# Optimization experiments

Measured on AMD Instinct MI355X. Metric: run time of the kernel, lower is better.

## Reference

```python
import jax, jax.numpy as jnp
import numpy as np

H = 128  # hidden_size hard-coded in the torch module


def _lin(key, fan_in, shape):
    b = 1.0 / np.sqrt(fan_in)
    return jax.random.uniform(key, shape, minval=-b, maxval=b, dtype=jnp.float32)


def _gru_step(x, wih, bih, bhh):
    # torch GRU, single time step, h0 = 0; gate order (r, z, n)
    g = x @ wih.T + bih
    xr, xz, xn = jnp.split(g, 3, axis=-1)
    br, bz, bn = jnp.split(bhh, 3)
    r = jax.nn.sigmoid(xr + br)
    z = jax.nn.sigmoid(xz + bz)
    n = jnp.tanh(xn + r * bn)
    return (1.0 - z) * n  # h' = (1-z)*n + z*0


def _forward(x_node, x_edge, nt_w1, nt_b1, nt_w2, nt_b2, et_w, et_b,
             ngru_wih, ngru_bih, ngru_bhh, egru_wih, egru_bih, egru_bhh,
             natt_w, natt_b, eatt_w, eatt_b,
             lr_w1, lr_b1, lr_w2, lr_b2, cr_w1, cr_b1, cr_w2, cr_b2,
             mr_w1, mr_b1, mr_w2, mr_b2, pairs):
    B, N, _ = x_node.shape
    node_f = jax.nn.relu(x_node @ nt_w1 + nt_b1) @ nt_w2 + nt_b2      # [B,N,H]
    edge_f = x_edge @ et_w + et_b                                      # [B,N,N,H]
    nh = eh = None
    for _ in range(2):  # num_time_steps; GRU inputs are NOT updated in the original loop
        nh = _gru_step(node_f, ngru_wih, ngru_bih, ngru_bhh)           # [B,N,H]
        eh = _gru_step(edge_f, egru_wih, egru_bih, egru_bhh)           # [B,N,N,H]
        # --- node message pooling: attention over column index j ---
        n_col = jnp.broadcast_to(nh[:, :, None, :], eh.shape)          # aug[b,i,j] = nh[b,i]
        logits = (jnp.concatenate([n_col, eh], -1) @ natt_w)[..., 0] + natt_b[0]
        w = jax.nn.softmax(logits, axis=-1)                            # [B,N,N]
        nh = jnp.einsum('bijk,bij->bik', eh, w)                        # pooled node states
        # --- edge message pooling: 2-way attention over (row, col) node states ---
        n_row = jnp.broadcast_to(nh[:, None, :, :], eh.shape)          # [b,i,j] = nh[b,j]
        n_col = jnp.broadcast_to(nh[:, :, None, :], eh.shape)          # [b,i,j] = nh[b,i]
        l_row = (jnp.concatenate([n_row, eh], -1) @ eatt_w)[..., 0] + eatt_b[0]
        l_col = (jnp.concatenate([n_col, eh], -1) @ eatt_w)[..., 0] + eatt_b[0]
        w2 = jax.nn.softmax(jnp.stack([l_row, l_col], -1), axis=-1)    # [B,N,N,2]
        eh = w2[..., 0:1] * n_row + w2[..., 1:2] * n_col               # einsum('bijl,bijkl->bijk')
    # --- classifier inputs (aggregator = elementwise mean) ---
    i0, i1 = pairs[..., 0], pairs[..., 1]                              # [B,P]
    emb0 = jnp.take_along_axis(nh, i0[..., None], axis=1)              # [B,P,H]
    emb1 = jnp.take_along_axis(nh, i1[..., None], axis=1)
    bix = jnp.arange(B)[:, None]
    e01 = eh[bix, i0, i1]                                              # [B,P,H]
    e10 = eh[bix, i1, i0]
    ci = jnp.concatenate([(emb0 + emb1) * 0.5, (e01 + e10) * 0.5], -1)  # [B,P,2H]

    def head(w1, b1, wo, bo):
        return jax.nn.relu(ci @ w1 + b1) @ wo + bo

    lr = head(lr_w1, lr_b1, lr_w2, lr_b2)
    cr = head(cr_w1, cr_b1, cr_w2, cr_b2)
    mr = head(mr_w1, mr_b1, mr_w2, mr_b2)
    return jnp.concatenate([lr, cr, mr], axis=-1)                      # [B,P,6+5+3]


def setup_inputs() -> dict:
    B, N, P = 16, 64, 128
    NF, EF = 1024, 512
    CH = 512  # classifier hidden
    ks = list(jax.random.split(jax.random.key(0), 40))
    k = iter(ks)
    inp = {}
    inp['concatenated_node_features'] = jax.random.normal(next(k), (B, N, NF), dtype=jnp.float32)
    inp['interaction_feature'] = jax.random.normal(next(k), (B, N, N, EF), dtype=jnp.float32)
    inp['nt_w1'] = _lin(next(k), NF, (NF, 512)); inp['nt_b1'] = _lin(next(k), NF, (512,))
    inp['nt_w2'] = _lin(next(k), 512, (512, H)); inp['nt_b2'] = _lin(next(k), 512, (H,))
    inp['et_w'] = _lin(next(k), EF, (EF, H)); inp['et_b'] = _lin(next(k), EF, (H,))
    inp['ngru_wih'] = _lin(next(k), H, (3 * H, H))
    inp['ngru_bih'] = _lin(next(k), H, (3 * H,)); inp['ngru_bhh'] = _lin(next(k), H, (3 * H,))
    inp['egru_wih'] = _lin(next(k), H, (3 * H, H))
    inp['egru_bih'] = _lin(next(k), H, (3 * H,)); inp['egru_bhh'] = _lin(next(k), H, (3 * H,))
    inp['natt_w'] = _lin(next(k), 2 * H, (2 * H, 1)); inp['natt_b'] = _lin(next(k), 2 * H, (1,))
    inp['eatt_w'] = _lin(next(k), 2 * H, (2 * H, 1)); inp['eatt_b'] = _lin(next(k), 2 * H, (1,))
    for name, od in (('lr', 6), ('cr', 5), ('mr', 3)):
        inp[name + '_w1'] = _lin(next(k), 2 * H, (2 * H, CH))
        inp[name + '_b1'] = _lin(next(k), 2 * H, (CH,))
        inp[name + '_w2'] = _lin(next(k), CH, (CH, od))
        inp[name + '_b2'] = _lin(next(k), CH, (od,))
    inp['object_pairs'] = jax.random.randint(next(k), (B, P, 2), 0, N, dtype=jnp.int64 if jax.config.jax_enable_x64 else jnp.int32)
    inp['num_relation'] = jax.random.randint(next(k), (B,), 0, P, dtype=jnp.int64 if jax.config.jax_enable_x64 else jnp.int32)
    return inp


def reference(concatenated_node_features, interaction_feature,
              nt_w1, nt_b1, nt_w2, nt_b2, et_w, et_b,
              ngru_wih, ngru_bih, ngru_bhh, egru_wih, egru_bih, egru_bhh,
              natt_w, natt_b, eatt_w, eatt_b,
              lr_w1, lr_b1, lr_w2, lr_b2, cr_w1, cr_b1, cr_w2, cr_b2,
              mr_w1, mr_b1, mr_w2, mr_b2, object_pairs, num_relation):
    # num_relation is read but unused in the original make_classifier_inputs loop
    return _forward(concatenated_node_features, interaction_feature,
                    nt_w1, nt_b1, nt_w2, nt_b2, et_w, et_b,
                    ngru_wih, ngru_bih, ngru_bhh, egru_wih, egru_bih, egru_bhh,
                    natt_w, natt_b, eatt_w, eatt_b,
                    lr_w1, lr_b1, lr_w2, lr_b2, cr_w1, cr_b1, cr_w2, cr_b2,
                    mr_w1, mr_b1, mr_w2, mr_b2, object_pairs)
```

## Files before the change

### kernel.cpp

```cpp
#include <hip/hip_runtime.h>
#include <math.h>
#include <stdint.h>


typedef __attribute__((ext_vector_type(8))) short short8;
typedef __attribute__((ext_vector_type(4))) float f32x4;

#define DEVINL __device__ __forceinline__

DEVINL float sigmoidf_(float x) { return 1.0f / (1.0f + __expf(-x)); }
DEVINL float tanhf_(float x) {
    float e = __expf(2.0f * x);
    return (e - 1.0f) / (e + 1.0f);
}
DEVINL short bf16_rne(float f) {
    uint32_t u = __float_as_uint(f);
    u += 0x7FFFu + ((u >> 16) & 1u);
    return (short)(u >> 16);
}
DEVINL float bf16_to_f(short s) {
    return __uint_as_float(((uint32_t)(uint16_t)s) << 16);
}
DEVINL void gload_lds16(const void* g, void* l) {
    __builtin_amdgcn_global_load_lds(
        (const __attribute__((address_space(1))) void*)(uintptr_t)g,
        (__attribute__((address_space(3))) void*)(uint32_t)(uintptr_t)l,
        16, 0, 0);
}
DEVINL void ldsbar() {
    asm volatile("s_waitcnt lgkmcnt(0)\n\ts_barrier" ::: "memory");
    __builtin_amdgcn_sched_barrier(0);
}

__global__ __launch_bounds__(256) void prep_all(
    const float* __restrict__ et_w, const float* __restrict__ wih,
    const float* __restrict__ w1a, const float* __restrict__ w1b,
    const float* __restrict__ w1c,
    short* __restrict__ Bf1, short* __restrict__ Bf2,
    short* __restrict__ Wf1_hi, short* __restrict__ Wf1_lo)
{
    const int bid = blockIdx.x, t = threadIdx.x;
    if (bid < 256) {
        int idx = bid * 256 + t;
        int k = idx >> 7, n = idx & 127;
        float v = et_w[(size_t)k * 128 + n];
        short hi = bf16_rne(v), lo = bf16_rne(v - bf16_to_f(hi));
        int kt = k >> 5, ct = n >> 4;
        int lane = (((k >> 3) & 3) << 4) | (n & 15);
        int j = k & 7;
        size_t s0 = ((((size_t)kt * 2 + 0) * 8 + ct) * 64 + lane) * 8 + j;
        size_t s1 = ((((size_t)kt * 2 + 1) * 8 + ct) * 64 + lane) * 8 + j;
        Bf1[s0] = hi; Bf1[s1] = lo;
    } else if (bid < 448) {
        int idx = (bid - 256) * 256 + t;
        int n = idx >> 7, k = idx & 127;
        float v = wih[(size_t)n * 128 + k];
        short hi = bf16_rne(v), lo = bf16_rne(v - bf16_to_f(hi));
        int kt = k >> 5, ct = n >> 4;
        int lane = (((k >> 3) & 3) << 4) | (n & 15);
        int j = k & 7;
        size_t s0 = ((((size_t)kt * 2 + 0) * 24 + ct) * 64 + lane) * 8 + j;
        size_t s1 = ((((size_t)kt * 2 + 1) * 24 + ct) * 64 + lane) * 8 + j;
        Bf2[s0] = hi; Bf2[s1] = lo;
    } else {
        int idx = (bid - 448) * 256 + t;
        int h = idx >> 17;
        int r = idx & 131071;
        int k = r >> 9, c = r & 511;
        const float* w1 = (h == 0) ? w1a : (h == 1) ? w1b : w1c;
        float v = w1[(size_t)k * 512 + c];
        short hi = bf16_rne(v), lo = bf16_rne(v - bf16_to_f(hi));
        int kt = k >> 5, ct = c >> 4;
        int lane = (((k >> 3) & 3) << 4) | (c & 15);
        int j = k & 7;
        size_t fidx = ((((size_t)h * 8 + kt) * 32 + ct) * 64 + lane) * 8 + j;
        Wf1_hi[fidx] = hi;
        Wf1_lo[fidx] = lo;
    }
}

#define PH1_ITER(KT, BH0, BH1, BL0, BL1, NBH0, NBH1, NBL0, NBL1,              \
                 PCV0, PCV1, PLD0, PLD1, RBUF, WBUF)                          \
    {                                                                         \
        if ((KT) < 15) {                                                      \
            const short* bkt = Bf1 + (size_t)((KT) + 1) * 8192;               \
            NBH0 = *(const short8*)(bkt + ct0 * 512 + ln8);                   \
            NBH1 = *(const short8*)(bkt + ct1 * 512 + ln8);                   \
            NBL0 = *(const short8*)(bkt + 4096 + ct0 * 512 + ln8);            \
            NBL1 = *(const short8*)(bkt + 4096 + ct1 * 512 + ln8);            \
            float av[8] = {PCV0.x, PCV0.y, PCV0.z, PCV0.w,                    \
                           PCV1.x, PCV1.y, PCV1.z, PCV1.w};                   \
            short8 h8, l8;                                                    \
            _Pragma("unroll") for (int j = 0; j < 8; ++j) {                   \
                short h = bf16_rne(av[j]);                                    \
                h8[j] = h;                                                    \
                l8[j] = bf16_rne(av[j] - bf16_to_f(h));                       \
            }                                                                 \
            *(short8*)(smem + (WBUF) + aslotb) = h8;                          \
            *(short8*)(smem + (WBUF) + 4096 + aslotb) = l8;                   \
        }                                                                     \
        if ((KT) < 14) {                                                      \
            PLD0 = *(const float4*)(aptr + (size_t)((KT) + 2) * 32);          \
            PLD1 = *(const float4*)(aptr + (size_t)((KT) + 2) * 32 + 4);      \
        }                                                                     \
        {                                                                     \
            const char* Ah_c = smem + (RBUF);                                 \
            short8 Ahf[4], Alf[4];                                            \
            _Pragma("unroll") for (int rt = 0; rt < 4; ++rt) {                \
                Ahf[rt] = *(const short8*)(Ah_c + (rt * 64 + lane) * 16);     \
                Alf[rt] = *(const short8*)(Ah_c + 4096 + (rt * 64 + lane) * 16); \
            }                                                                 \
            _Pragma("unroll") for (int rt = 0; rt < 4; ++rt) {                \
                acc1[rt][0] = __builtin_amdgcn_mfma_f32_16x16x32_bf16(Ahf[rt], BH0, acc1[rt][0], 0, 0, 0); \
                acc1[rt][0] = __builtin_amdgcn_mfma_f32_16x16x32_bf16(Alf[rt], BH0, acc1[rt][0], 0, 0, 0); \
                acc1[rt][0] = __builtin_amdgcn_mfma_f32_16x16x32_bf16(Ahf[rt], BL0, acc1[rt][0], 0, 0, 0); \
                acc1[rt][1] = __builtin_amdgcn_mfma_f32_16x16x32_bf16(Ahf[rt], BH1, acc1[rt][1], 0, 0, 0); \
                acc1[rt][1] = __builtin_amdgcn_mfma_f32_16x16x32_bf16(Alf[rt], BH1, acc1[rt][1], 0, 0, 0); \
                acc1[rt][1] = __builtin_amdgcn_mfma_f32_16x16x32_bf16(Ahf[rt], BL1, acc1[rt][1], 0, 0, 0); \
            }                                                                 \
        }                                                                     \
        ldsbar();                                                             \
    }

__global__ __launch_bounds__(256, 2) void fused_kernel(
    const float* __restrict__ x_edge,
    const short* __restrict__ Bf1, const short* __restrict__ Bf2,
    const float* __restrict__ et_b,
    const float* __restrict__ bih, const float* __restrict__ bhh,
    const float* __restrict__ natt_w, const float* __restrict__ eatt_w,
    float* __restrict__ nh_p, float* __restrict__ u_out)
{
    __shared__ __align__(16) char smem[81920];
    const int t = threadIdx.x;
    const int wv = t >> 6, lane = t & 63;
    const int g = blockIdx.x;
    const size_t bm = (size_t)g * 64;

    const int arow = t >> 2, akb = t & 3;
    const int aslotb = (((arow >> 4) * 64) + ((akb << 4) | (arow & 15))) * 16;
    const float* aptr = x_edge + (bm + arow) * 512 + akb * 8;

    const int ct0 = wv * 2, ct1 = wv * 2 + 1;
    const int ln8 = lane * 8;

    f32x4 acc1[4][2] = {};

    float4 paA0, paA1, paB0, paB1;
    short8 bhA0, bhA1, blA0, blA1, bhB0, bhB1, blB0, blB1;

    paA0 = *(const float4*)(aptr);
    paA1 = *(const float4*)(aptr + 4);
    paB0 = *(const float4*)(aptr + 32);
    paB1 = *(const float4*)(aptr + 36);
    {
        const short* bkt = Bf1;
        bhA0 = *(const short8*)(bkt + ct0 * 512 + ln8);
        bhA1 = *(const short8*)(bkt + ct1 * 512 + ln8);
        blA0 = *(const short8*)(bkt + 4096 + ct0 * 512 + ln8);
        blA1 = *(const short8*)(bkt + 4096 + ct1 * 512 + ln8);
    }
    {
        float av[8] = {paA0.x, paA0.y, paA0.z, paA0.w,
                       paA1.x, paA1.y, paA1.z, paA1.w};
        short8 h8, l8;
#pragma unroll
        for (int j = 0; j < 8; ++j) {
            short h = bf16_rne(av[j]);
            h8[j] = h;
            l8[j] = bf16_rne(av[j] - bf16_to_f(h));
        }
        *(short8*)(smem + aslotb) = h8;
        *(short8*)(smem + 4096 + aslotb) = l8;
    }
    ldsbar();

    for (int kt = 0; kt < 16; kt += 2) {
        PH1_ITER(kt, bhA0, bhA1, blA0, blA1, bhB0, bhB1, blB0, blB1,
                 paB0, paB1, paA0, paA1, 0, 8192)
        PH1_ITER(kt + 1, bhB0, bhB1, blB0, blB1, bhA0, bhA1, blA0, blA1,
                 paA0, paA1, paB0, paB1, 8192, 0)
    }
    __syncthreads();

    float* ef_s = (float*)smem;
#pragma unroll
    for (int c = 0; c < 2; ++c) {
        int col = wv * 32 + c * 16 + (lane & 15);
        float bias = et_b[col];
#pragma unroll
        for (int rt = 0; rt < 4; ++rt) {
#pragma unroll
            for (int q = 0; q < 4; ++q) {
                int row = rt * 16 + ((lane >> 4) << 2) + q;
                ef_s[row * 132 + col] = acc1[rt][c][q] + bias;
            }
        }
    }
    __syncthreads();

    short* AF = (short*)(smem + 49152);
#pragma unroll
    for (int u2 = 0; u2 < 4; ++u2) {
        int unit = t + u2 * 256;
        int kt2 = unit >> 8;
        int rt = (unit >> 6) & 3;
        int ln = unit & 63;
        int row = rt * 16 + (ln & 15);
        int feat0 = kt2 * 32 + (ln >> 4) * 8;
        const float* src = ef_s + row * 132 + feat0;
        float4 v0 = *(const float4*)(src);
        float4 v1 = *(const float4*)(src + 4);
        float av[8] = {v0.x, v0.y, v0.z, v0.w, v1.x, v1.y, v1.z, v1.w};
        short8 h8, l8;
#pragma unroll
        for (int j = 0; j < 8; ++j) {
            short hh = bf16_rne(av[j]);
            h8[j] = hh;
            l8[j] = bf16_rne(av[j] - bf16_to_f(hh));
        }
        *(short8*)(AF + (((kt2 * 2 + 0) * 4 + rt) * 64 + ln) * 8) = h8;
        *(short8*)(AF + (((kt2 * 2 + 1) * 4 + rt) * 64 + ln) * 8) = l8;
    }
    __syncthreads();

    f32x4 acc[4][6] = {};
    for (int kt = 0; kt < 4; ++kt) {
        {
            const char* src = (const char*)Bf2 + (size_t)kt * 49152;
#pragma unroll
            for (int i = 0; i < 12; ++i) {
                int off = (t + i * 256) * 16;
                gload_lds16(src + off, smem + off);
            }
        }
        __syncthreads();

        const char* Ab = (const char*)AF + kt * 8192;
        short8 Ahf[4], Alf[4];
#pragma unroll
        for (int rt = 0; rt < 4; ++rt) {
            Ahf[rt] = *(const short8*)(Ab + (rt * 64 + lane) * 16);
            Alf[rt] = *(const short8*)(Ab + 4096 + (rt * 64 + lane) * 16);
        }
#pragma unroll
        for (int c = 0; c < 6; ++c) {
            int ctg = ((c >> 1) << 3) + (wv << 1) + (c & 1);
            short8 Bh = *(const short8*)(smem + (ctg * 64 + lane) * 16);
            short8 Bl = *(const short8*)(smem + 24576 + (ctg * 64 + lane) * 16);
#pragma unroll
            for (int rt = 0; rt < 4; ++rt) {
                acc[rt][c] = __builtin_amdgcn_mfma_f32_16x16x32_bf16(Ahf[rt], Bh, acc[rt][c], 0, 0, 0);
                acc[rt][c] = __builtin_amdgcn_mfma_f32_16x16x32_bf16(Alf[rt], Bh, acc[rt][c], 0, 0, 0);
                acc[rt][c] = __builtin_amdgcn_mfma_f32_16x16x32_bf16(Ahf[rt], Bl, acc[rt][c], 0, 0, 0);
            }
        }
        __syncthreads();
    }

    const int EHP = 132;
    float* eh_s = (float*)smem;
    float* red  = (float*)(smem + 33792);
    float* s2v  = red + 256;
    float* ewv  = s2v + 64;
#pragma unroll
    for (int cc = 0; cc < 2; ++cc) {
        int o = (wv << 5) + (cc << 4) + (lane & 15);
        float bco = bih[o] + bhh[o];
        float bcz = bih[128 + o] + bhh[128 + o];
        float bcn = bih[256 + o];
        float bn3 = bhh[256 + o];
#pragma unroll
        for (int rt = 0; rt < 4; ++rt) {
#pragma unroll
            for (int q = 0; q < 4; ++q) {
                int row = rt * 16 + ((lane >> 4) << 2) + q;
                float r = sigmoidf_(acc[rt][cc][q] + bco);
                float z = sigmoidf_(acc[rt][2 + cc][q] + bcz);
                float n = tanhf_(acc[rt][4 + cc][q] + bcn + r * bn3);
                eh_s[row * EHP + o] = (1.0f - z) * n;
            }
        }
    }
    __syncthreads();

    {
        int j = t >> 2, q = t & 3;
        const float* row = eh_s + j * EHP + q * 32;
        const float* wb = natt_w + 128 + q * 32;
        float a = 0.f;
#pragma unroll
        for (int k2 = 0; k2 < 32; ++k2) a = fmaf(row[k2], wb[k2], a);
        red[t] = a;
    }
    __syncthreads();
    if (t < 64) s2v[t] = red[4 * t] + red[4 * t + 1] + red[4 * t + 2] + red[4 * t + 3];
    __syncthreads();
    if (t < 64) {
        float m = -1e30f;
        for (int j = 0; j < 64; ++j) m = fmaxf(m, s2v[j]);
        ewv[t] = __expf(s2v[t] - m);
    }
    __syncthreads();
    float inv = 0.f;
    for (int j = 0; j < 64; ++j) inv += ewv[j];
    inv = 1.0f / inv;
    {
        int o = t & 127, h = t >> 7;
        float a = 0.f;
        for (int j = h * 32; j < h * 32 + 32; ++j)
            a = fmaf(ewv[j], eh_s[j * EHP + o], a);
        __syncthreads();
        red[t] = a;
    }
    __syncthreads();
    if (t < 128) {
        float v = (red[t] + red[t + 128]) * inv;
        nh_p[(size_t)g * 128 + t] = v;
        red[t] = v * eatt_w[t];
    }
    __syncthreads();
    for (int s = 64; s > 0; s >>= 1) {
        if (t < s) red[t] += red[t + s];
        __syncthreads();
    }
    if (t == 0) u_out[g] = red[0];
}

__global__ __launch_bounds__(128) void ci_kernel(
    const float* __restrict__ nh_p, const float* __restrict__ u,
    const int* __restrict__ pairs, float* __restrict__ ci)
{
    const int bp = blockIdx.x;
    const int b  = bp >> 7;
    const int t  = threadIdx.x;
    int i0 = pairs[bp * 2 + 0];
    int i1 = pairs[bp * 2 + 1];
    const float* n0 = nh_p + (size_t)(b * 64 + i0) * 128;
    const float* n1 = nh_p + (size_t)(b * 64 + i1) * 128;
    float s = sigmoidf_(u[b * 64 + i1] - u[b * 64 + i0]);
    float v0 = n0[t], v1 = n1[t];
    ci[(size_t)bp * 256 + t]       = 0.5f * (v0 + v1);
    ci[(size_t)bp * 256 + 128 + t] = s * v1 + (1.0f - s) * v0;
}

__global__ __launch_bounds__(256, 1) void headcls_kernel(
    const float* __restrict__ ci,
    const short* __restrict__ Wf1_hi, const short* __restrict__ Wf1_lo,
    const float* __restrict__ b1a, const float* __restrict__ b1b,
    const float* __restrict__ b1c,
    const float* __restrict__ w2a, const float* __restrict__ w2b,
    const float* __restrict__ w2c,
    const float* __restrict__ b2a, const float* __restrict__ b2b,
    const float* __restrict__ b2c,
    float* __restrict__ out)
{
    __shared__ __align__(16) char smem[139264];
    const int t = threadIdx.x;
    const int wv = t >> 6, lane = t & 63;
    const int rb = blockIdx.x;
    const int hd = blockIdx.y;
    const float* b1 = hd == 0 ? b1a : hd == 1 ? b1b : b1c;
    const float* w2 = hd == 0 ? w2a : hd == 1 ? w2b : w2c;
    const float* b2 = hd == 0 ? b2a : hd == 1 ? b2b : b2c;
    const int od  = hd == 0 ? 6 : hd == 1 ? 5 : 3;
    const int off = hd == 0 ? 0 : hd == 1 ? 6 : 11;

    const int arow = t >> 2, akb = t & 3;
    const int abyte = ((((arow >> 4) * 64) + ((akb << 4) | (arow & 15))) * 8) * 2;
    const float* aptr = ci + ((size_t)rb * 32 + arow) * 256 + akb * 8;

    f32x4 acc[2][8] = {};

    float4 a0, a1;
    if (t < 128) {
        a0 = *(const float4*)(aptr);
        a1 = *(const float4*)(aptr + 4);
    }
    {
        const char* sh = (const char*)(Wf1_hi + (size_t)hd * 8 * 32 * 512);
        const char* sl = (const char*)(Wf1_lo + (size_t)hd * 8 * 32 * 512);
#pragma unroll
        for (int i = 0; i < 8; ++i) {
            int ch = i * 4 + wv;
            int o2 = ch * 1024 + lane * 16;
            gload_lds16(sh + o2, smem + ch * 1024);
            gload_lds16(sl + o2, smem + 32768 + ch * 1024);
        }
    }
    if (t < 128) {
        float av[8] = {a0.x, a0.y, a0.z, a0.w, a1.x, a1.y, a1.z, a1.w};
        short8 h8, l8;
#pragma unroll
        for (int j = 0; j < 8; ++j) {
            short h = bf16_rne(av[j]);
            h8[j] = h;
            l8[j] = bf16_rne(av[j] - bf16_to_f(h));
        }
        *(short8*)(smem + 131072 + abyte) = h8;
        *(short8*)(smem + 131072 + 2048 + abyte) = l8;
    }
    __syncthreads();

    for (int kt = 0; kt < 8; ++kt) {
        const int cur = kt & 1;
        const char* Bh_c = smem + cur * 65536;
        const char* Bl_c = Bh_c + 32768;
        const char* Ah_c = smem + 131072 + cur * 4096;
        const char* Al_c = Ah_c + 2048;

        float4 b0, b1v;
        if (kt < 7) {
            const char* sh = (const char*)(Wf1_hi + ((size_t)hd * 8 + kt + 1) * 32 * 512);
            const char* sl = (const char*)(Wf1_lo + ((size_t)hd * 8 + kt + 1) * 32 * 512);
            char* dBh = smem + (cur ^ 1) * 65536;
#pragma unroll
            for (int i = 0; i < 8; ++i) {
                int ch = i * 4 + wv;
                int o2 = ch * 1024 + lane * 16;
                gload_lds16(sh + o2, dBh + ch * 1024);
                gload_lds16(sl + o2, dBh + 32768 + ch * 1024);
            }
            if (t < 128) {
                b0  = *(const float4*)(aptr + (size_t)(kt + 1) * 32);
                b1v = *(const float4*)(aptr + (size_t)(kt + 1) * 32 + 4);
            }
        }

        short8 Ah[2], Al[2];
#pragma unroll
        for (int rt = 0; rt < 2; ++rt) {
            Ah[rt] = *(const short8*)(Ah_c + (rt * 64 + lane) * 16);
            Al[rt] = *(const short8*)(Al_c + (rt * 64 + lane) * 16);
        }
#pragma unroll
        for (int c = 0; c < 8; ++c) {
            int ctg = wv * 8 + c;
            short8 Bh = *(const short8*)(Bh_c + (ctg * 64 + lane) * 16);
            short8 Bl = *(const short8*)(Bl_c + (ctg * 64 + lane) * 16);
#pragma unroll
            for (int rt = 0; rt < 2; ++rt) {
                acc[rt][c] = __builtin_amdgcn_mfma_f32_16x16x32_bf16(Ah[rt], Bh, acc[rt][c], 0, 0, 0);
                acc[rt][c] = __builtin_amdgcn_mfma_f32_16x16x32_bf16(Al[rt], Bh, acc[rt][c], 0, 0, 0);
                acc[rt][c] = __builtin_amdgcn_mfma_f32_16x16x32_bf16(Ah[rt], Bl, acc[rt][c], 0, 0, 0);
            }
        }

        if (kt < 7 && t < 128) {
            float av[8] = {b0.x, b0.y, b0.z, b0.w, b1v.x, b1v.y, b1v.z, b1v.w};
            short8 h8, l8;
#pragma unroll
            for (int j = 0; j < 8; ++j) {
                short h = bf16_rne(av[j]);
                h8[j] = h;
                l8[j] = bf16_rne(av[j] - bf16_to_f(h));
            }
            char* dAh = smem + 131072 + (cur ^ 1) * 4096;
            *(short8*)(dAh + abyte) = h8;
            *(short8*)(dAh + 2048 + abyte) = l8;
        }
        __syncthreads();
    }

    float* h_s  = (float*)smem;
    float* w2_s = (float*)(smem + 66048);
    for (int idx = t; idx < 512 * od; idx += 256) w2_s[idx] = w2[idx];
#pragma unroll
    for (int c = 0; c < 8; ++c) {
        int ctg = wv * 8 + c;
        int col = ctg * 16 + (lane & 15);
        float bias = b1[col];
#pragma unroll
        for (int rt = 0; rt < 2; ++rt) {
#pragma unroll
            for (int q = 0; q < 4; ++q) {
                int row = rt * 16 + ((lane >> 4) << 2) + q;
                h_s[row * 516 + col] = fmaxf(acc[rt][c][q] + bias, 0.f);
            }
        }
    }
    __syncthreads();

    {
        int row = t >> 3, o = t & 7;
        if (o < od) {
            const float* hr = h_s + row * 516;
            float a = b2[o];
            for (int c = 0; c < 512; ++c)
                a = fmaf(hr[c], w2_s[c * od + o], a);
            out[((size_t)rb * 32 + row) * 14 + off + o] = a;
        }
    }
}

extern "C" void kernel_launch(void* const* d_in, const int* in_sizes, int n_in,
                              void* d_out, int out_size, void* d_ws, size_t ws_size,
                              hipStream_t stream)
{
    const float* x_edge   = (const float*)d_in[1];
    const float* et_w     = (const float*)d_in[6];
    const float* et_b     = (const float*)d_in[7];
    const float* egru_wih = (const float*)d_in[11];
    const float* egru_bih = (const float*)d_in[12];
    const float* egru_bhh = (const float*)d_in[13];
    const float* natt_w   = (const float*)d_in[14];
    const float* eatt_w   = (const float*)d_in[16];
    const float* lr_w1 = (const float*)d_in[18];
    const float* lr_b1 = (const float*)d_in[19];
    const float* lr_w2 = (const float*)d_in[20];
    const float* lr_b2 = (const float*)d_in[21];
    const float* cr_w1 = (const float*)d_in[22];
    const float* cr_b1 = (const float*)d_in[23];
    const float* cr_w2 = (const float*)d_in[24];
    const float* cr_b2 = (const float*)d_in[25];
    const float* mr_w1 = (const float*)d_in[26];
    const float* mr_b1 = (const float*)d_in[27];
    const float* mr_w2 = (const float*)d_in[28];
    const float* mr_b2 = (const float*)d_in[29];
    const int* pairs   = (const int*)d_in[30];
    float* out = (float*)d_out;
    char* ws = (char*)d_ws;

    short* Bf1    = (short*)(ws + 0);
    short* Bf2    = (short*)(ws + 262144);
    short* Wf1_hi = (short*)(ws + 458752);
    short* Wf1_lo = (short*)(ws + 1245184);
    float* nh_p   = (float*)(ws + 2031616);
    float* u      = (float*)(ws + 2555904);
    float* ci     = (float*)(ws + 2560000);

    prep_all<<<1984, 256, 0, stream>>>(et_w, egru_wih, lr_w1, cr_w1, mr_w1,
                                       Bf1, Bf2, Wf1_hi, Wf1_lo);

    fused_kernel<<<1024, 256, 0, stream>>>(
        x_edge, Bf1, Bf2, et_b, egru_bih, egru_bhh, natt_w, eatt_w, nh_p, u);

    ci_kernel<<<2048, 128, 0, stream>>>(nh_p, u, pairs, ci);

    headcls_kernel<<<dim3(64, 3), 256, 0, stream>>>(
        ci, Wf1_hi, Wf1_lo, lr_b1, cr_b1, mr_b1,
        lr_w2, cr_w2, mr_w2, lr_b2, cr_b2, mr_b2, out);
}
```

Baseline: 93.33 us.

## Shrink LDS footprint to raise occupancy; read GRU weights directly from global

Shared memory drops from 80 KB to about 48.5 KB and launch bounds go from 2 to 3 blocks per CU, so more blocks can be resident at once. To fit, the edge-feature staging to bf16 hi/lo fragments is done in two 32-row halves, and the second GEMM now loads its B fragments straight from global (L2) into registers instead of staging them through LDS. That removes per-k-tile barriers but adds global-load latency on the MFMA path. The tighter register budget that comes with 3 blocks per CU may cause spills given the large accumulator arrays.

```diff
diff --git a/kernel.cpp b/kernel.cpp
--- a/kernel.cpp
+++ b/kernel.cpp
@@ -122,7 +122,7 @@
         ldsbar();                                                             \
     }
 
-__global__ __launch_bounds__(256, 2) void fused_kernel(
+__global__ __launch_bounds__(256, 3) void fused_kernel(
     const float* __restrict__ x_edge,
     const short* __restrict__ Bf1, const short* __restrict__ Bf2,
     const float* __restrict__ et_b,
@@ -130,7 +130,7 @@
     const float* __restrict__ natt_w, const float* __restrict__ eatt_w,
     float* __restrict__ nh_p, float* __restrict__ u_out)
 {
-    __shared__ __align__(16) char smem[81920];
+    __shared__ __align__(16) char smem[49664];
     const int t = threadIdx.x;
     const int wv = t >> 6, lane = t & 63;
     const int g = blockIdx.x;
@@ -180,82 +180,104 @@
         PH1_ITER(kt + 1, bhB0, bhB1, blB0, blB1, bhA0, bhA1, blA0, blA1,
                  paA0, paA1, paB0, paB1, 8192, 0)
     }
-    __syncthreads();
-
-    float* ef_s = (float*)smem;
-#pragma unroll
-    for (int c = 0; c < 2; ++c) {
-        int col = wv * 32 + c * 16 + (lane & 15);
-        float bias = et_b[col];
-#pragma unroll
-        for (int rt = 0; rt < 4; ++rt) {
-#pragma unroll
-            for (int q = 0; q < 4; ++q) {
-                int row = rt * 16 + ((lane >> 4) << 2) + q;
-                ef_s[row * 132 + col] = acc1[rt][c][q] + bias;
-            }
-        }
-    }
-    __syncthreads();
-
-    short* AF = (short*)(smem + 49152);
-#pragma unroll
-    for (int u2 = 0; u2 < 4; ++u2) {
-        int unit = t + u2 * 256;
-        int kt2 = unit >> 8;
-        int rt = (unit >> 6) & 3;
-        int ln = unit & 63;
-        int row = rt * 16 + (ln & 15);
-        int feat0 = kt2 * 32 + (ln >> 4) * 8;
-        const float* src = ef_s + row * 132 + feat0;
-        float4 v0 = *(const float4*)(src);
-        float4 v1 = *(const float4*)(src + 4);
-        float av[8] = {v0.x, v0.y, v0.z, v0.w, v1.x, v1.y, v1.z, v1.w};
-        short8 h8, l8;
-#pragma unroll
-        for (int j = 0; j < 8; ++j) {
-            short hh = bf16_rne(av[j]);
-            h8[j] = hh;
-            l8[j] = bf16_rne(av[j] - bf16_to_f(hh));
-        }
-        *(short8*)(AF + (((kt2 * 2 + 0) * 4 + rt) * 64 + ln) * 8) = h8;
-        *(short8*)(AF + (((kt2 * 2 + 1) * 4 + rt) * 64 + ln) * 8) = l8;
+
+    float* ef_h = (float*)smem;
+    short* AF = (short*)(smem + 16896);
+#pragma unroll
+    for (int h = 0; h < 2; ++h) {
+        __syncthreads();
+#pragma unroll
+        for (int c = 0; c < 2; ++c) {
+            int col = wv * 32 + c * 16 + (lane & 15);
+            float bias = et_b[col];
+#pragma unroll
+            for (int rr = 0; rr < 2; ++rr) {
+                int rt = 2 * h + rr;
+#pragma unroll
+                for (int q = 0; q < 4; ++q) {
+                    int lrow = rr * 16 + ((lane >> 4) << 2) + q;
+                    ef_h[lrow * 132 + col] = acc1[rt][c][q] + bias;
+                }
+            }
+        }
+        __syncthreads();
+#pragma unroll
+        for (int p = 0; p < 2; ++p) {
+            int unit = t + p * 256;
+            int kt2 = unit >> 7;
+            int rr = (unit >> 6) & 1;
+            int ln = unit & 63;
+            int rt = 2 * h + rr;
+            int lrow = rr * 16 + (ln & 15);
+            int feat0 = kt2 * 32 + (ln >> 4) * 8;
+            const float* src = ef_h + lrow * 132 + feat0;
+            float4 v0 = *(const float4*)(src);
+            float4 v1 = *(const float4*)(src + 4);
+            float av[8] = {v0.x, v0.y, v0.z, v0.w, v1.x, v1.y, v1.z, v1.w};
+            short8 h8, l8;
+#pragma unroll
+            for (int j = 0; j < 8; ++j) {
+                short hh = bf16_rne(av[j]);
+                h8[j] = hh;
+                l8[j] = bf16_rne(av[j] - bf16_to_f(hh));
+            }
+            *(short8*)(AF + (((kt2 * 2 + 0) * 4 + rt) * 64 + ln) * 8) = h8;
+            *(short8*)(AF + (((kt2 * 2 + 1) * 4 + rt) * 64 + ln) * 8) = l8;
+        }
     }
     __syncthreads();
 
     f32x4 acc[4][6] = {};
+#pragma unroll
     for (int kt = 0; kt < 4; ++kt) {
+        const short* bkt = Bf2 + (size_t)kt * 24576;
+        const char* Ab = (const char*)AF + kt * 8192;
         {
-            const char* src = (const char*)Bf2 + (size_t)kt * 49152;
-#pragma unroll
-            for (int i = 0; i < 12; ++i) {
-                int off = (t + i * 256) * 16;
-                gload_lds16(src + off, smem + off);
-            }
-        }
-        __syncthreads();
-
-        const char* Ab = (const char*)AF + kt * 8192;
-        short8 Ahf[4], Alf[4];
-#pragma unroll
-        for (int rt = 0; rt < 4; ++rt) {
-            Ahf[rt] = *(const short8*)(Ab + (rt * 64 + lane) * 16);
-            Alf[rt] = *(const short8*)(Ab + 4096 + (rt * 64 + lane) * 16);
-        }
-#pragma unroll
-        for (int c = 0; c < 6; ++c) {
-            int ctg = ((c >> 1) << 3) + (wv << 1) + (c & 1);
-            short8 Bh = *(const short8*)(smem + (ctg * 64 + lane) * 16);
-            short8 Bl = *(const short8*)(smem + 24576 + (ctg * 64 + lane) * 16);
-#pragma unroll
-            for (int rt = 0; rt < 4; ++rt) {
-                acc[rt][c] = __builtin_amdgcn_mfma_f32_16x16x32_bf16(Ahf[rt], Bh, acc[rt][c], 0, 0, 0);
-                acc[rt][c] = __builtin_amdgcn_mfma_f32_16x16x32_bf16(Alf[rt], Bh, acc[rt][c], 0, 0, 0);
-                acc[rt][c] = __builtin_amdgcn_mfma_f32_16x16x32_bf16(Ahf[rt], Bl, acc[rt][c], 0, 0, 0);
-            }
-        }
-        __syncthreads();
-    }
+            short8 Bh[6];
+#pragma unroll
+            for (int c = 0; c < 6; ++c) {
+                int ctg = ((c >> 1) << 3) + (wv << 1) + (c & 1);
+                Bh[c] = *(const short8*)(bkt + ctg * 512 + ln8);
+            }
+#pragma unroll
+            for (int rtp = 0; rtp < 2; ++rtp) {
+                short8 Ah[2], Al[2];
+#pragma unroll
+                for (int r = 0; r < 2; ++r) {
+                    Ah[r] = *(const short8*)(Ab + ((rtp * 2 + r) * 64 + lane) * 16);
+                    Al[r] = *(const short8*)(Ab + 4096 + ((rtp * 2 + r) * 64 + lane) * 16);
+                }
+#pragma unroll
+                for (int c = 0; c < 6; ++c)
+#pragma unroll
+                    for (int r = 0; r < 2; ++r) {
+                        acc[rtp * 2 + r][c] = __builtin_amdgcn_mfma_f32_16x16x32_bf16(Ah[r], Bh[c], acc[rtp * 2 + r][c], 0, 0, 0);
+                        acc[rtp * 2 + r][c] = __builtin_amdgcn_mfma_f32_16x16x32_bf16(Al[r], Bh[c], acc[rtp * 2 + r][c], 0, 0, 0);
+                    }
+            }
+        }
+        {
+            short8 Bl[6];
+#pragma unroll
+            for (int c = 0; c < 6; ++c) {
+                int ctg = ((c >> 1) << 3) + (wv << 1) + (c & 1);
+                Bl[c] = *(const short8*)(bkt + 12288 + ctg * 512 + ln8);
+            }
+#pragma unroll
+            for (int rtp = 0; rtp < 2; ++rtp) {
+                short8 Ah[2];
+#pragma unroll
+                for (int r = 0; r < 2; ++r)
+                    Ah[r] = *(const short8*)(Ab + ((rtp * 2 + r) * 64 + lane) * 16);
+#pragma unroll
+                for (int c = 0; c < 6; ++c)
+#pragma unroll
+                    for (int r = 0; r < 2; ++r)
+                        acc[rtp * 2 + r][c] = __builtin_amdgcn_mfma_f32_16x16x32_bf16(Ah[r], Bl[c], acc[rtp * 2 + r][c], 0, 0, 0);
+            }
+        }
+    }
+    __syncthreads();
 
     const int EHP = 132;
     float* eh_s = (float*)smem;
```

New measurement: 92.40 us. Within noise of the previous version (-1.0%).

## Shrink LDS and read GRU weights from global to raise occupancy

Applied to the files above, without the earlier changes.

Removes the LDS staging of the bf16 hi/lo A fragments and of the Bf2 weight tiles. A fragments are now converted from the fp32 edge-feature tile on the fly, and B fragments are read straight from global memory (cache). This cuts static shared memory from 80KB to about 34.5KB and raises launch_bounds to 4 blocks per CU, removing per-k-tile barriers. In exchange, the B fragments are re-read from global by each row-tile pair, the hi/lo conversion is redone for every k-step, and the tighter register budget under the higher launch bound can cause spills.

```diff
diff --git a/kernel.cpp b/kernel.cpp
--- a/kernel.cpp
+++ b/kernel.cpp
@@ -122,7 +122,7 @@
         ldsbar();                                                             \
     }
 
-__global__ __launch_bounds__(256, 2) void fused_kernel(
+__global__ __launch_bounds__(256, 4) void fused_kernel(
     const float* __restrict__ x_edge,
     const short* __restrict__ Bf1, const short* __restrict__ Bf2,
     const float* __restrict__ et_b,
@@ -130,7 +130,7 @@
     const float* __restrict__ natt_w, const float* __restrict__ eatt_w,
     float* __restrict__ nh_p, float* __restrict__ u_out)
 {
-    __shared__ __align__(16) char smem[81920];
+    __shared__ __align__(16) char smem[35328];
     const int t = threadIdx.x;
     const int wv = t >> 6, lane = t & 63;
     const int g = blockIdx.x;
@@ -198,64 +198,44 @@
     }
     __syncthreads();
 
-    short* AF = (short*)(smem + 49152);
-#pragma unroll
-    for (int u2 = 0; u2 < 4; ++u2) {
-        int unit = t + u2 * 256;
-        int kt2 = unit >> 8;
-        int rt = (unit >> 6) & 3;
-        int ln = unit & 63;
-        int row = rt * 16 + (ln & 15);
-        int feat0 = kt2 * 32 + (ln >> 4) * 8;
-        const float* src = ef_s + row * 132 + feat0;
-        float4 v0 = *(const float4*)(src);
-        float4 v1 = *(const float4*)(src + 4);
-        float av[8] = {v0.x, v0.y, v0.z, v0.w, v1.x, v1.y, v1.z, v1.w};
-        short8 h8, l8;
-#pragma unroll
-        for (int j = 0; j < 8; ++j) {
-            short hh = bf16_rne(av[j]);
-            h8[j] = hh;
-            l8[j] = bf16_rne(av[j] - bf16_to_f(hh));
-        }
-        *(short8*)(AF + (((kt2 * 2 + 0) * 4 + rt) * 64 + ln) * 8) = h8;
-        *(short8*)(AF + (((kt2 * 2 + 1) * 4 + rt) * 64 + ln) * 8) = l8;
-    }
-    __syncthreads();
-
     f32x4 acc[4][6] = {};
+#pragma unroll
     for (int kt = 0; kt < 4; ++kt) {
-        {
-            const char* src = (const char*)Bf2 + (size_t)kt * 49152;
-#pragma unroll
-            for (int i = 0; i < 12; ++i) {
-                int off = (t + i * 256) * 16;
-                gload_lds16(src + off, smem + off);
-            }
-        }
-        __syncthreads();
-
-        const char* Ab = (const char*)AF + kt * 8192;
-        short8 Ahf[4], Alf[4];
-#pragma unroll
-        for (int rt = 0; rt < 4; ++rt) {
-            Ahf[rt] = *(const short8*)(Ab + (rt * 64 + lane) * 16);
-            Alf[rt] = *(const short8*)(Ab + 4096 + (rt * 64 + lane) * 16);
-        }
-#pragma unroll
-        for (int c = 0; c < 6; ++c) {
-            int ctg = ((c >> 1) << 3) + (wv << 1) + (c & 1);
-            short8 Bh = *(const short8*)(smem + (ctg * 64 + lane) * 16);
-            short8 Bl = *(const short8*)(smem + 24576 + (ctg * 64 + lane) * 16);
-#pragma unroll
-            for (int rt = 0; rt < 4; ++rt) {
-                acc[rt][c] = __builtin_amdgcn_mfma_f32_16x16x32_bf16(Ahf[rt], Bh, acc[rt][c], 0, 0, 0);
-                acc[rt][c] = __builtin_amdgcn_mfma_f32_16x16x32_bf16(Alf[rt], Bh, acc[rt][c], 0, 0, 0);
-                acc[rt][c] = __builtin_amdgcn_mfma_f32_16x16x32_bf16(Ahf[rt], Bl, acc[rt][c], 0, 0, 0);
-            }
-        }
-        __syncthreads();
-    }
+        const short* bkt = Bf2 + (size_t)kt * 24576;
+#pragma unroll
+        for (int rtp = 0; rtp < 2; ++rtp) {
+            short8 Ah[2], Al[2];
+#pragma unroll
+            for (int r = 0; r < 2; ++r) {
+                int rt = rtp * 2 + r;
+                const float* src = ef_s + (rt * 16 + (lane & 15)) * 132
+                                 + kt * 32 + (lane >> 4) * 8;
+                float4 v0 = *(const float4*)(src);
+                float4 v1 = *(const float4*)(src + 4);
+                float av[8] = {v0.x, v0.y, v0.z, v0.w, v1.x, v1.y, v1.z, v1.w};
+#pragma unroll
+                for (int j = 0; j < 8; ++j) {
+                    short hh = bf16_rne(av[j]);
+                    Ah[r][j] = hh;
+                    Al[r][j] = bf16_rne(av[j] - bf16_to_f(hh));
+                }
+            }
+#pragma unroll
+            for (int c = 0; c < 6; ++c) {
+                int ctg = ((c >> 1) << 3) + (wv << 1) + (c & 1);
+                short8 Bh = *(const short8*)(bkt + ctg * 512 + ln8);
+                short8 Bl = *(const short8*)(bkt + 12288 + ctg * 512 + ln8);
+#pragma unroll
+                for (int r = 0; r < 2; ++r) {
+                    int rt = rtp * 2 + r;
+                    acc[rt][c] = __builtin_amdgcn_mfma_f32_16x16x32_bf16(Ah[r], Bh, acc[rt][c], 0, 0, 0);
+                    acc[rt][c] = __builtin_amdgcn_mfma_f32_16x16x32_bf16(Al[r], Bh, acc[rt][c], 0, 0, 0);
+                    acc[rt][c] = __builtin_amdgcn_mfma_f32_16x16x32_bf16(Ah[r], Bl, acc[rt][c], 0, 0, 0);
+                }
+            }
+        }
+    }
+    __syncthreads();
 
     const int EHP = 132;
     float* eh_s = (float*)smem;
```

New measurement: 196.9 us. +111.0%, slower.
